# Kernel optimization log

Hardware: AMD Instinct MI355X
Metric: run time of the kernel (lower is better)

Reference implementation:

```python
import jax, jax.numpy as jnp
import numpy as np

P = 10          # num_vars (agents)
DIM = 2         # out_dims (2D)
K = 5           # order
H = 256         # hidden_layer_size
INPUT_DIM = 40  # per-agent feature block
ND = DIM + (P - 1) * DIM  # num_dims_model = 20
OUT = ND * DIM            # per-net MLP output = 40
T = 20000


def _gather_idx():
    # per-agent selected features: [pos(dim), relpos (p-1)*dim] (skips vel at offset dim..2*dim)
    base = np.arange(P) * INPUT_DIM
    a = np.arange(DIM)[None, :] + base[:, None]                      # (P, dim)
    b = np.arange(2 * DIM, (2 + P - 1) * DIM)[None, :] + base[:, None]  # (P, (p-1)*dim)
    return np.concatenate([a, b], axis=1)  # (P, ND)


def _fp_idx():
    i = np.arange(P)[:, None]
    j = np.arange(P - 1)[None, :]
    indd = (i + 1) * INPUT_DIM - (P - 1) + j        # last (p-1) entries of block i
    indd2 = indd - (P - 1)                          # preceding (p-1) entries
    return indd, indd2


def setup_inputs() -> dict:
    key = jax.random.key(0)
    ks = jax.random.split(key, 8)
    s = 0.05
    return {
        "inputs": jax.random.normal(ks[0], (T, K, P * INPUT_DIM), dtype=jnp.float32),
        "W1": jax.random.normal(ks[1], (K, P, ND, H), dtype=jnp.float32) * s,
        "b1": jnp.zeros((K, P, H), dtype=jnp.float32),
        "W2": jax.random.normal(ks[2], (K, P, H, H), dtype=jnp.float32) * s,
        "b2": jnp.zeros((K, P, H), dtype=jnp.float32),
        "W3": jax.random.normal(ks[3], (K, P, H, OUT), dtype=jnp.float32) * s,
        "b3": jnp.zeros((K, P, OUT), dtype=jnp.float32),
        "avoid": jnp.asarray(0.1, dtype=jnp.float32),  # avoid_nets.bias (bat init)
    }


def reference(inputs, W1, b1, W2, b2, W3, b3, avoid):
    Tl = inputs.shape[0]
    idx = _gather_idx()
    indd, indd2 = _fp_idx()

    # pairwise perceptual gating, 'bat' branch (uses avoid bias)
    xlast = inputs[:, -1, :]                       # (T, P*INPUT_DIM)
    xF = xlast[:, indd]                            # (T, P, P-1)
    xF2 = xlast[:, indd2]                          # (T, P, P-1)
    coeffs_FP = jax.nn.sigmoid(100.0 * (xF - avoid)) * (jax.nn.sigmoid(100.0 * xF2) - 0.5) * 2.0

    # grouped per-(k,i) MLPs, batched via einsum
    sel = inputs[:, :, idx]                        # (T, K, P, ND)
    h = jax.nn.relu(jnp.einsum('tkpn,kpnh->tkph', sel, W1) + b1)
    h = jax.nn.relu(jnp.einsum('tkph,kphg->tkpg', h, W2) + b2)
    c = jnp.einsum('tkpg,kpgo->tkpo', h, W3) + b3  # (T, K, P, OUT)
    c = (c ** 2).reshape(Tl, K, P, DIM, ND)        # percept: squared coeffs

    # gate last (p-1)*dim coefficient columns by coeffs_FP (repeated dim times)
    gate = jnp.repeat(coeffs_FP, DIM, axis=-1)     # (T, P, (P-1)*DIM)
    mult = jnp.concatenate([jnp.ones((Tl, P, DIM), dtype=c.dtype), gate], axis=-1)  # (T, P, ND)
    c2 = c * mult[:, None, :, None, :]             # (T, K, P, DIM, ND)

    preds = jnp.einsum('tkpon,tkpn->tpo', c2, sel).reshape(Tl, P * DIM)
    coeffs = c2.reshape(Tl, K, P * DIM, ND)
    return preds, coeffs, coeffs_FP
```

## Files before the change

kernel.cpp:

```cpp
#include <hip/hip_runtime.h>
#include <hip/hip_bf16.h>

#define Kn   5
#define Pn   10
#define Hn   256
#define NDn  20
#define OUTn 40
#define INDn 40
#define ROWn 400
#define TT   32
#define CSTRIDE 52

typedef float  f32x4  __attribute__((ext_vector_type(4)));
typedef float  f32x2  __attribute__((ext_vector_type(2)));
typedef short  bf16x8 __attribute__((ext_vector_type(8)));
typedef unsigned int u32;
typedef unsigned short u16;

#define W1B_OFF 0
#define W1B_PER 8192
#define W2B_OFF 409600
#define W2B_PER 65536
#define W3B_OFF 3686400
#define W3B_PER 12288
#define WS_ELEMS 4300800
#define WS_BYTES (WS_ELEMS * 2)

__device__ __forceinline__ u16 f2bf(float f) {
    u32 u = __float_as_uint(f);
    return (u16)((u + 0x7fffu + ((u >> 16) & 1u)) >> 16);
}

__device__ __forceinline__ u32 cvt_pk_bf16(float a, float b) {
    u32 r;
    asm("v_cvt_pk_bf16_f32 %0, %1, %2" : "=v"(r) : "v"(a), "v"(b));
    return r;
}

__global__ void prep_weights(const float* __restrict__ W1, const float* __restrict__ W2,
                             const float* __restrict__ W3, const float* __restrict__ inputs,
                             const float* __restrict__ avoid_p,
                             float* __restrict__ cfp, short* __restrict__ ws, int T) {
    int sid = blockIdx.x * 256 + threadIdx.x;
    const float* src; int e, kst, n, ss, kmax, ng, nmax; size_t obase;
    if (sid < 51200) {
        e = sid >> 10; int r = sid & 1023; n = r >> 2; ss = r & 3; kst = 0;
        src = W1 + (size_t)e * (NDn * Hn); kmax = NDn; ng = Hn; nmax = Hn;
        obase = W1B_OFF + (size_t)e * W1B_PER;
    } else if (sid < 460800) {
        int s = sid - 51200; e = s >> 13; int r = s & 8191;
        kst = r >> 10; int rr = r & 1023; n = rr >> 2; ss = rr & 3;
        src = W2 + (size_t)e * (Hn * Hn); kmax = Hn; ng = Hn; nmax = Hn;
        obase = W2B_OFF + (size_t)e * W2B_PER + (size_t)kst * 8192;
    } else if (sid < 537600) {
        int s = sid - 460800; e = s / 1536; int r = s - e * 1536;
        kst = r / 192; int rr = r - kst * 192; n = rr >> 2; ss = rr & 3;
        src = W3 + (size_t)e * (Hn * OUTn); kmax = Hn; ng = OUTn; nmax = OUTn;
        obase = W3B_OFF + (size_t)e * W3B_PER + (size_t)kst * 1536;
    } else {
        int g = sid - 537600;
        if (g < T * (Pn * (Pn - 1))) {
            int t = g / 90, rm = g - t * 90;
            int pp = rm / 9, j = rm - pp * 9;
            size_t base = ((size_t)t * Kn + (Kn - 1)) * ROWn + pp * INDn;
            float xF  = inputs[base + 31 + j];
            float xF2 = inputs[base + 22 + j];
            float s1 = 1.0f / (1.0f + __expf(-100.0f * (xF - *avoid_p)));
            float s2 = 1.0f / (1.0f + __expf(-100.0f * xF2));
            cfp[g] = s1 * (s2 - 0.5f) * 2.0f;
        }
        return;
    }

    u16 v[8];
    #pragma unroll
    for (int j = 0; j < 8; ++j) {
        int k = kst * 32 + ss * 8 + j;
        float f = (k < kmax && n < nmax) ? src[(size_t)k * ng + n] : 0.0f;
        v[j] = f2bf(f);
    }
    u32 q0 = (u32)v[0] | ((u32)v[1] << 16), q1 = (u32)v[2] | ((u32)v[3] << 16);
    u32 q2 = (u32)v[4] | ((u32)v[5] << 16), q3 = (u32)v[6] | ((u32)v[7] << 16);
    *(uint4*)(ws + obase + (size_t)n * 32 + ss * 8) = make_uint4(q0, q1, q2, q3);
}

__device__ __forceinline__ void epi_store_h(short* hA_, const f32x4 (*A)[4],
                                            int wid, int lane) {
    const int lg = lane >> 4, lr = lane & 15;
    #pragma unroll
    for (int mt = 0; mt < 2; ++mt) {
        #pragma unroll
        for (int r = 0; r < 4; ++r) {
            const int t = 16 * mt + 4 * lg + r;
            #pragma unroll
            for (int nt = 0; nt < 4; ++nt) {
                float vv = fmaxf(A[mt][nt][r], 0.0f);
                u32 pk = cvt_pk_bf16(vv, vv);
                int col = 64 * wid + 16 * nt + lr;
                int off = t * 512 + ((2 * col) ^ ((t & 7) << 4));
                *reinterpret_cast<u16*>(reinterpret_cast<char*>(hA_) + off) = (u16)pk;
            }
        }
    }
}

template<int KS>
__device__ __forceinline__ void c_step(const char* w2, const short* hA_, int wid,
                                       int lg, int lr, bf16x8 (&cur)[4], bf16x8 (&nxt)[4],
                                       f32x4 (&acc)[2][4]) {
    if (KS < 7) {
        #pragma unroll
        for (int nt = 0; nt < 4; ++nt) {
            int n = 64 * wid + 16 * nt + lr;
            nxt[nt] = *(const bf16x8*)(w2 + (KS + 1) * 16384 + n * 64 + lg * 16);
        }
    }
    bf16x8 aF[2];
    #pragma unroll
    for (int mt = 0; mt < 2; ++mt) {
        int t = 16 * mt + lr;
        aF[mt] = *(const bf16x8*)((const char*)hA_ + t * 512 + ((KS * 64 + lg * 16) ^ ((t & 7) << 4)));
    }
    #pragma unroll
    for (int mt = 0; mt < 2; ++mt)
        #pragma unroll
        for (int nt = 0; nt < 4; ++nt)
            acc[mt][nt] = __builtin_amdgcn_mfma_f32_16x16x32_bf16(aF[mt], cur[nt], acc[mt][nt], 0, 0, 0);
}

template<int KS>
__device__ __forceinline__ void d_step(const char* w3, const short* hA_, int t, int ncnt,
                                       int nbase, int lg, int lr,
                                       bf16x8 (&cur)[2], bf16x8 (&nxt)[2], f32x4 (&accd)[2]) {
    if (KS < 7) {
        #pragma unroll
        for (int j = 0; j < 2; ++j)
            if (j < ncnt) {
                int n = 16 * (nbase + j) + lr;
                nxt[j] = *(const bf16x8*)(w3 + (KS + 1) * 3072 + n * 64 + lg * 16);
            }
    }
    bf16x8 aF = *(const bf16x8*)((const char*)hA_ + t * 512 + ((KS * 64 + lg * 16) ^ ((t & 7) << 4)));
    #pragma unroll
    for (int j = 0; j < 2; ++j)
        if (j < ncnt)
            accd[j] = __builtin_amdgcn_mfma_f32_16x16x32_bf16(aF, cur[j], accd[j], 0, 0, 0);
}

__launch_bounds__(256, 4)
__global__ void senngc_mfma(const float* __restrict__ inputs,
                            const float* __restrict__ b1, const float* __restrict__ b2,
                            const float* __restrict__ b3,
                            const float* __restrict__ cfp_in,
                            const short* __restrict__ ws,
                            float* __restrict__ preds, float* __restrict__ coeffs, int T)
{
    __shared__ __align__(16) short selA[TT * 32];
    __shared__ __align__(16) short hA[TT * Hn];
    __shared__ u16  sh_mult[TT][NDn];

    const int tid  = threadIdx.x;

    const int NB   = gridDim.x;
    const int nch  = NB / (Pn * Kn);
    const int bx   = blockIdx.x & 7, bj = blockIdx.x >> 3;
    const int bbase = NB >> 3, brem = NB & 7;
    const int L    = bx * bbase + (bx < brem ? bx : brem) + bj;
    const int pair = L / nch;
    const int t0   = (L - pair * nch) * TT;
    const int p    = pair / Kn;
    const int ke   = pair - p * Kn;

    const int wid  = tid >> 6, lane = tid & 63;
    const int lg   = lane >> 4, lr = lane & 15;

    const int e = ke * Pn + p;
    const char* w1 = (const char*)(ws + W1B_OFF + (size_t)e * W1B_PER);
    const char* w2 = (const char*)(ws + W2B_OFF + (size_t)e * W2B_PER);
    const char* w3 = (const char*)(ws + W3B_OFF + (size_t)e * W3B_PER);

    if (tid < 128) {
        int row = tid >> 2, ss = tid & 3;
        int kg = ss ^ ((row >> 1) & 3);
        int trow = (t0 + row < T) ? (t0 + row) : (T - 1);
        const float* src = inputs + ((size_t)trow * Kn + ke) * ROWn + p * INDn;
        int c0 = kg ? (kg * 8 + 2) : 0;
        int o1 = kg ? (c0 + 2) : 4;
        int o2 = kg ? (c0 + 4) : 6;
        int o3 = kg ? (c0 + 6) : 8;
        f32x2 va = *(const f32x2*)(src + c0);
        f32x2 vb = *(const f32x2*)(src + o1);
        f32x2 vc = *(const f32x2*)(src + o2);
        f32x2 vd = *(const f32x2*)(src + o3);
        float f[8] = {va[0], va[1], vb[0], vb[1], vc[0], vc[1], vd[0], vd[1]};
        #pragma unroll
        for (int j = 0; j < 8; ++j)
            if (kg * 8 + j >= NDn) f[j] = 0.0f;
        u32 q0 = cvt_pk_bf16(f[0], f[1]), q1 = cvt_pk_bf16(f[2], f[3]);
        u32 q2 = cvt_pk_bf16(f[4], f[5]), q3 = cvt_pk_bf16(f[6], f[7]);
        *(uint4*)((char*)selA + row * 64 + ss * 16) = make_uint4(q0, q1, q2, q3);
    }

    if (tid < 32) *(u32*)&sh_mult[tid][0] = 0x3F803F80u;
    {
        int r = tid / 9, j = tid - r * 9;
        if (tid < TT * (Pn - 1)) {
            float cf = (t0 + r < T) ? cfp_in[(size_t)(t0 + r) * (Pn * (Pn - 1)) + p * (Pn - 1) + j] : 0.0f;
            *(u32*)&sh_mult[r][2 + 2 * j] = cvt_pk_bf16(cf, cf);
        }
        int i2 = tid + 256;
        if (i2 < TT * (Pn - 1)) {
            int r2 = i2 / 9, j2 = i2 - r2 * 9;
            float cf = (t0 + r2 < T) ? cfp_in[(size_t)(t0 + r2) * (Pn * (Pn - 1)) + p * (Pn - 1) + j2] : 0.0f;
            *(u32*)&sh_mult[r2][2 + 2 * j2] = cvt_pk_bf16(cf, cf);
        }
    }

    bf16x8 bW[4];
    float bias1[4], bias2[4];
    #pragma unroll
    for (int nt = 0; nt < 4; ++nt) {
        int n = 64 * wid + 16 * nt + lr;
        bW[nt] = *(const bf16x8*)(w1 + n * 64 + lg * 16);
        bias1[nt] = b1[e * Hn + n];
        bias2[nt] = b2[e * Hn + n];
    }
    __syncthreads();

    f32x4 acc[2][4];

    #pragma unroll
    for (int mt = 0; mt < 2; ++mt)
        #pragma unroll
        for (int nt = 0; nt < 4; ++nt)
            acc[mt][nt] = (f32x4){bias1[nt], bias1[nt], bias1[nt], bias1[nt]};
    {
        bf16x8 aS[2];
        #pragma unroll
        for (int mt = 0; mt < 2; ++mt) {
            int t = 16 * mt + lr;
            aS[mt] = *(const bf16x8*)((const char*)selA + t * 64 + ((lg ^ ((t >> 1) & 3)) << 4));
        }
        #pragma unroll
        for (int mt = 0; mt < 2; ++mt)
            #pragma unroll
            for (int nt = 0; nt < 4; ++nt)
                acc[mt][nt] = __builtin_amdgcn_mfma_f32_16x16x32_bf16(aS[mt], bW[nt], acc[mt][nt], 0, 0, 0);
    }
    bf16x8 bA[4], bB[4];
    #pragma unroll
    for (int nt = 0; nt < 4; ++nt) {
        int n = 64 * wid + 16 * nt + lr;
        bA[nt] = *(const bf16x8*)(w2 + n * 64 + lg * 16);
    }
    epi_store_h(hA, acc, wid, lane);
    __syncthreads();

    #pragma unroll
    for (int mt = 0; mt < 2; ++mt)
        #pragma unroll
        for (int nt = 0; nt < 4; ++nt)
            acc[mt][nt] = (f32x4){bias2[nt], bias2[nt], bias2[nt], bias2[nt]};
    c_step<0>(w2, hA, wid, lg, lr, bA, bB, acc);
    c_step<1>(w2, hA, wid, lg, lr, bB, bA, acc);
    c_step<2>(w2, hA, wid, lg, lr, bA, bB, acc);
    c_step<3>(w2, hA, wid, lg, lr, bB, bA, acc);
    c_step<4>(w2, hA, wid, lg, lr, bA, bB, acc);
    c_step<5>(w2, hA, wid, lg, lr, bB, bA, acc);
    c_step<6>(w2, hA, wid, lg, lr, bA, bB, acc);
    c_step<7>(w2, hA, wid, lg, lr, bB, bA, acc);
    __syncthreads();

    const int mslot = wid >> 1;
    const int nbase = (wid & 1) ? 2 : 0;
    const int ncnt  = (wid & 1) ? 1 : 2;
    const int tD    = 16 * mslot + lr;
    bf16x8 dA[2], dB[2];
    #pragma unroll
    for (int j = 0; j < 2; ++j)
        if (j < ncnt) {
            int n = 16 * (nbase + j) + lr;
            dA[j] = *(const bf16x8*)(w3 + n * 64 + lg * 16);
        }
    epi_store_h(hA, acc, wid, lane);
    __syncthreads();

    {
        f32x4 accd[2];
        accd[0] = (f32x4){0.f, 0.f, 0.f, 0.f};
        accd[1] = (f32x4){0.f, 0.f, 0.f, 0.f};
        d_step<0>(w3, hA, tD, ncnt, nbase, lg, lr, dA, dB, accd);
        d_step<1>(w3, hA, tD, ncnt, nbase, lg, lr, dB, dA, accd);
        d_step<2>(w3, hA, tD, ncnt, nbase, lg, lr, dA, dB, accd);
        d_step<3>(w3, hA, tD, ncnt, nbase, lg, lr, dB, dA, accd);
        d_step<4>(w3, hA, tD, ncnt, nbase, lg, lr, dA, dB, accd);
        d_step<5>(w3, hA, tD, ncnt, nbase, lg, lr, dB, dA, accd);
        d_step<6>(w3, hA, tD, ncnt, nbase, lg, lr, dA, dB, accd);
        d_step<7>(w3, hA, tD, ncnt, nbase, lg, lr, dB, dA, accd);
        __syncthreads();
        {
            float* cst = (float*)hA;
            #pragma unroll
            for (int j = 0; j < 2; ++j)
                if (j < ncnt)
                    #pragma unroll
                    for (int r = 0; r < 4; ++r)
                        cst[(16 * mslot + 4 * lg + r) * CSTRIDE + 16 * (nbase + j) + lr] = accd[j][r];
        }
    }
    __syncthreads();

    {
        const float* cst = (const float*)hA;
        const int r  = tid >> 3, g = tid & 7;
        const int d  = g >> 2;
        const int o0 = 5 * g;
        const int n0 = 5 * (g & 3);
        float s = 0.0f;
        if (t0 + r < T) {
            const float* bb3 = b3 + e * OUTn + o0;
            float* crow = coeffs + (((size_t)(t0 + r) * Kn + ke) * Pn + p) * OUTn + o0;
            #pragma unroll
            for (int j = 0; j < 5; ++j) {
                float c = cst[r * CSTRIDE + o0 + j] + bb3[j];
                int n = n0 + j;
                float m = __uint_as_float((u32)sh_mult[r][n] << 16);
                float c2 = c * c * m;
                crow[j] = c2;
                int offs = r * 64 + (((n >> 3) ^ ((r >> 1) & 3)) << 4) + (n & 7) * 2;
                u16 u = *(const u16*)((const char*)selA + offs);
                s = fmaf(c2, __uint_as_float((u32)u << 16), s);
            }
        }
        s += __shfl_xor(s, 1);
        s += __shfl_xor(s, 2);
        if ((g & 3) == 0 && t0 + r < T)
            atomicAdd(&preds[(size_t)(t0 + r) * (Pn * 2) + p * 2 + d], s);
    }
}

#define FMA4(ACC, A, W)              \
    ACC.x = fmaf(A.x, W, ACC.x);     \
    ACC.y = fmaf(A.y, W, ACC.y);     \
    ACC.z = fmaf(A.z, W, ACC.z);     \
    ACC.w = fmaf(A.w, W, ACC.w);

__launch_bounds__(256, 4)
__global__ void senngc_fused_f32(const float* __restrict__ inputs,
                                 const float* __restrict__ W1, const float* __restrict__ b1,
                                 const float* __restrict__ W2, const float* __restrict__ b2,
                                 const float* __restrict__ W3, const float* __restrict__ b3,
                                 const float* __restrict__ avoid_p,
                                 float* __restrict__ preds, float* __restrict__ coeffs,
                                 float* __restrict__ cfp, int T)
{
    __shared__ __align__(16) float lds_T[Hn * 32];
    __shared__ __align__(16) float selT[NDn * 32];
    __shared__ float sh_mult[32][NDn];
    __shared__ float sh_pred[32][2];

    const int tid = threadIdx.x;
    const int p   = blockIdx.y;
    const int t0  = blockIdx.x * 32;
    const float avoid = *avoid_p;

    if (tid < 64) {
        sh_pred[tid >> 1][tid & 1] = 0.0f;
        sh_mult[tid >> 1][tid & 1] = 1.0f;
    }
    for (int i = tid; i < 32 * (Pn - 1); i += 256) {
        int r = i / 9, j = i - r * 9;
        float cf = 0.0f;
        if (t0 + r < T) {
            size_t base = ((size_t)(t0 + r) * Kn + (Kn - 1)) * ROWn + p * INDn;
            float xF  = inputs[base + 31 + j];
            float xF2 = inputs[base + 22 + j];
            float s1 = 1.0f / (1.0f + __expf(-100.0f * (xF - avoid)));
            float s2 = 1.0f / (1.0f + __expf(-100.0f * xF2));
            cf = s1 * (s2 - 0.5f) * 2.0f;
            cfp[(size_t)(t0 + r) * (Pn * (Pn - 1)) + p * (Pn - 1) + j] = cf;
        }
        sh_mult[r][2 + 2 * j] = cf;
        sh_mult[r][3 + 2 * j] = cf;
    }

    const int tr = tid >> 5;
    const int tc = tid & 31;
    float4 acc[8];

    for (int k = 0; k < Kn; ++k) {
        __syncthreads();
        for (int i = tid; i < NDn * 32; i += 256) {
            int n = i >> 5, r = i & 31;
            float v = 0.0f;
            if (t0 + r < T) {
                int col = p * INDn + (n < 2 ? n : n + 2);
                v = inputs[((size_t)(t0 + r) * Kn + k) * ROWn + col];
            }
            selT[n * 32 + r] = v;
        }
        __syncthreads();
        {
            const float* w1 = W1 + (size_t)(k * Pn + p) * NDn * Hn;
            const float* bb = b1 + (k * Pn + p) * Hn;
            float4 bv0 = *(const float4*)(bb + 8 * tc);
            float4 bv1 = *(const float4*)(bb + 8 * tc + 4);
            acc[0] = make_float4(bv0.x, bv0.x, bv0.x, bv0.x);
            acc[1] = make_float4(bv0.y, bv0.y, bv0.y, bv0.y);
            acc[2] = make_float4(bv0.z, bv0.z, bv0.z, bv0.z);
            acc[3] = make_float4(bv0.w, bv0.w, bv0.w, bv0.w);
            acc[4] = make_float4(bv1.x, bv1.x, bv1.x, bv1.x);
            acc[5] = make_float4(bv1.y, bv1.y, bv1.y, bv1.y);
            acc[6] = make_float4(bv1.z, bv1.z, bv1.z, bv1.z);
            acc[7] = make_float4(bv1.w, bv1.w, bv1.w, bv1.w);
            #pragma unroll 4
            for (int kk = 0; kk < NDn; ++kk) {
                float4 a = *(const float4*)&selT[kk * 32 + 4 * tr];
                const float* wr = w1 + kk * Hn + 8 * tc;
                float4 w0  = *(const float4*)(wr);
                float4 w1v = *(const float4*)(wr + 4);
                FMA4(acc[0], a, w0.x);  FMA4(acc[1], a, w0.y);
                FMA4(acc[2], a, w0.z);  FMA4(acc[3], a, w0.w);
                FMA4(acc[4], a, w1v.x); FMA4(acc[5], a, w1v.y);
                FMA4(acc[6], a, w1v.z); FMA4(acc[7], a, w1v.w);
            }
            #pragma unroll
            for (int c = 0; c < 8; ++c) {
                int col = 8 * tc + c;
                float4 v = acc[c];
                v.x = fmaxf(v.x, 0.0f); v.y = fmaxf(v.y, 0.0f);
                v.z = fmaxf(v.z, 0.0f); v.w = fmaxf(v.w, 0.0f);
                *(float4*)&lds_T[col * 32 + ((4 * tr) ^ ((col & 7) << 2))] = v;
            }
        }
        __syncthreads();
        {
            const float* w2 = W2 + (size_t)(k * Pn + p) * Hn * Hn;
            const float* bb = b2 + (k * Pn + p) * Hn;
            float4 bv0 = *(const float4*)(bb + 8 * tc);
            float4 bv1 = *(const float4*)(bb + 8 * tc + 4);
            acc[0] = make_float4(bv0.x, bv0.x, bv0.x, bv0.x);
            acc[1] = make_float4(bv0.y, bv0.y, bv0.y, bv0.y);
            acc[2] = make_float4(bv0.z, bv0.z, bv0.z, bv0.z);
            acc[3] = make_float4(bv0.w, bv0.w, bv0.w, bv0.w);
            acc[4] = make_float4(bv1.x, bv1.x, bv1.x, bv1.x);
            acc[5] = make_float4(bv1.y, bv1.y, bv1.y, bv1.y);
            acc[6] = make_float4(bv1.z, bv1.z, bv1.z, bv1.z);
            acc[7] = make_float4(bv1.w, bv1.w, bv1.w, bv1.w);
            #pragma unroll 2
            for (int kk = 0; kk < Hn; ++kk) {
                float4 a = *(const float4*)&lds_T[kk * 32 + ((4 * tr) ^ ((kk & 7) << 2))];
                const float* wr = w2 + kk * Hn + 8 * tc;
                float4 w0  = *(const float4*)(wr);
                float4 w1v = *(const float4*)(wr + 4);
                FMA4(acc[0], a, w0.x);  FMA4(acc[1], a, w0.y);
                FMA4(acc[2], a, w0.z);  FMA4(acc[3], a, w0.w);
                FMA4(acc[4], a, w1v.x); FMA4(acc[5], a, w1v.y);
                FMA4(acc[6], a, w1v.z); FMA4(acc[7], a, w1v.w);
            }
            __syncthreads();
            #pragma unroll
            for (int c = 0; c < 8; ++c) {
                int col = 8 * tc + c;
                float4 v = acc[c];
                v.x = fmaxf(v.x, 0.0f); v.y = fmaxf(v.y, 0.0f);
                v.z = fmaxf(v.z, 0.0f); v.w = fmaxf(v.w, 0.0f);
                *(float4*)&lds_T[col * 32 + ((4 * tr) ^ ((col & 7) << 2))] = v;
            }
        }
        __syncthreads();
        {
            const int kq  = tid >> 6;
            const int tr2 = (tid >> 3) & 7;
            const int cg  = tid & 7;
            const float* w3 = W3 + (size_t)(k * Pn + p) * Hn * OUTn;
            float accd[4][5];
            #pragma unroll
            for (int a_ = 0; a_ < 4; ++a_)
                #pragma unroll
                for (int j = 0; j < 5; ++j) accd[a_][j] = 0.0f;
            #pragma unroll 2
            for (int kk = kq * 64; kk < kq * 64 + 64; ++kk) {
                float4 a = *(const float4*)&lds_T[kk * 32 + ((4 * tr2) ^ ((kk & 7) << 2))];
                const float* wr = w3 + kk * OUTn + 5 * cg;
                #pragma unroll
                for (int j = 0; j < 5; ++j) {
                    float w = wr[j];
                    accd[0][j] = fmaf(a.x, w, accd[0][j]);
                    accd[1][j] = fmaf(a.y, w, accd[1][j]);
                    accd[2][j] = fmaf(a.z, w, accd[2][j]);
                    accd[3][j] = fmaf(a.w, w, accd[3][j]);
                }
            }
            __syncthreads();
            #pragma unroll
            for (int r4 = 0; r4 < 4; ++r4)
                #pragma unroll
                for (int j = 0; j < 5; ++j)
                    lds_T[(kq * 32 + 4 * tr2 + r4) * OUTn + 5 * cg + j] = accd[r4][j];
        }
        __syncthreads();
        {
            const float* bb3 = b3 + (k * Pn + p) * OUTn;
            for (int i = tid; i < 32 * OUTn; i += 256) {
                int r = i / OUTn, o = i - r * OUTn;
                if (t0 + r >= T) continue;
                float c = bb3[o]
                        + lds_T[(0 * 32 + r) * OUTn + o]
                        + lds_T[(1 * 32 + r) * OUTn + o]
                        + lds_T[(2 * 32 + r) * OUTn + o]
                        + lds_T[(3 * 32 + r) * OUTn + o];
                int d = (o >= NDn) ? 1 : 0;
                int n = o - d * NDn;
                float c2 = c * c * sh_mult[r][n];
                coeffs[(((size_t)(t0 + r) * Kn + k) * Pn + p) * OUTn + o] = c2;
                atomicAdd(&sh_pred[r][d], c2 * selT[n * 32 + r]);
            }
        }
    }

    __syncthreads();
    if (tid < 64) {
        int r = tid >> 1, d = tid & 1;
        if (t0 + r < T)
            preds[(size_t)(t0 + r) * (Pn * 2) + p * 2 + d] = sh_pred[r][d];
    }
}

extern "C" void kernel_launch(void* const* d_in, const int* in_sizes, int n_in,
                              void* d_out, int out_size, void* d_ws, size_t ws_size,
                              hipStream_t stream) {
    const float* inputs = (const float*)d_in[0];
    const float* W1 = (const float*)d_in[1];
    const float* b1 = (const float*)d_in[2];
    const float* W2 = (const float*)d_in[3];
    const float* b2 = (const float*)d_in[4];
    const float* W3 = (const float*)d_in[5];
    const float* b3 = (const float*)d_in[6];
    const float* avoid = (const float*)d_in[7];
    const int T = in_sizes[0] / (Kn * ROWn);

    float* out    = (float*)d_out;
    float* preds  = out;
    float* coeffs = out + (size_t)T * (Pn * 2);
    float* cfp    = coeffs + (size_t)T * Kn * Pn * OUTn;

    if (ws_size >= (size_t)WS_BYTES) {
        short* ws = (short*)d_ws;
        hipMemsetAsync(preds, 0, (size_t)T * (Pn * 2) * sizeof(float), stream);
        const int prep_items = 537600 + T * (Pn * (Pn - 1));
        hipLaunchKernelGGL(prep_weights, dim3((prep_items + 255) / 256), dim3(256), 0, stream,
                           W1, W2, W3, inputs, avoid, cfp, ws, T);
        const int nch = (T + TT - 1) / TT;
        hipLaunchKernelGGL(senngc_mfma, dim3(nch * Pn * Kn), dim3(256), 0, stream,
                           inputs, b1, b2, b3, cfp, ws, preds, coeffs, T);
    } else {
        dim3 grid((T + 31) / 32, Pn);
        hipLaunchKernelGGL(senngc_fused_f32, grid, dim3(256), 0, stream,
                           inputs, W1, b1, W2, b2, W3, b3, avoid, preds, coeffs, cfp, T);
    }
}
```

Measured before the change: 445.9 us.

## Double time tile to 64 rows with 8 waves sharing each weight load

Raises the per-block time tile from 32 to 64 rows and the block from 256 to 512 threads. The 8 waves are split into two row halves and four column quarters, so each block's weight slices are used for twice as many rows and the number of blocks is halved. This is meant to cut redundant W1/W2/W3 global/L2 traffic per output row. In exchange it doubles shared memory for hA and selA, which may lower occupancy, and the layer-3/epilogue wave mapping (mslot = wid>>1) was not visibly updated for 8 waves.

```diff
diff --git a/kernel.cpp b/kernel.cpp
--- a/kernel.cpp
+++ b/kernel.cpp
@@ -8,7 +8,7 @@
 #define OUTn 40
 #define INDn 40
 #define ROWn 400
-#define TT   32
+#define TT   64
 #define CSTRIDE 52
 
 typedef float  f32x4  __attribute__((ext_vector_type(4)));
@@ -85,18 +85,18 @@
 }
 
 __device__ __forceinline__ void epi_store_h(short* hA_, const f32x4 (*A)[4],
-                                            int wid, int lane) {
+                                            int mh, int nq, int lane) {
     const int lg = lane >> 4, lr = lane & 15;
     #pragma unroll
     for (int mt = 0; mt < 2; ++mt) {
         #pragma unroll
         for (int r = 0; r < 4; ++r) {
-            const int t = 16 * mt + 4 * lg + r;
+            const int t = 32 * mh + 16 * mt + 4 * lg + r;
             #pragma unroll
             for (int nt = 0; nt < 4; ++nt) {
                 float vv = fmaxf(A[mt][nt][r], 0.0f);
                 u32 pk = cvt_pk_bf16(vv, vv);
-                int col = 64 * wid + 16 * nt + lr;
+                int col = 64 * nq + 16 * nt + lr;
                 int off = t * 512 + ((2 * col) ^ ((t & 7) << 4));
                 *reinterpret_cast<u16*>(reinterpret_cast<char*>(hA_) + off) = (u16)pk;
             }
@@ -105,20 +105,20 @@
 }
 
 template<int KS>
-__device__ __forceinline__ void c_step(const char* w2, const short* hA_, int wid,
+__device__ __forceinline__ void c_step(const char* w2, const short* hA_, int mh, int nq,
                                        int lg, int lr, bf16x8 (&cur)[4], bf16x8 (&nxt)[4],
                                        f32x4 (&acc)[2][4]) {
     if (KS < 7) {
         #pragma unroll
         for (int nt = 0; nt < 4; ++nt) {
-            int n = 64 * wid + 16 * nt + lr;
+            int n = 64 * nq + 16 * nt + lr;
             nxt[nt] = *(const bf16x8*)(w2 + (KS + 1) * 16384 + n * 64 + lg * 16);
         }
     }
     bf16x8 aF[2];
     #pragma unroll
     for (int mt = 0; mt < 2; ++mt) {
-        int t = 16 * mt + lr;
+        int t = 32 * mh + 16 * mt + lr;
         aF[mt] = *(const bf16x8*)((const char*)hA_ + t * 512 + ((KS * 64 + lg * 16) ^ ((t & 7) << 4)));
     }
     #pragma unroll
@@ -147,7 +147,7 @@
             accd[j] = __builtin_amdgcn_mfma_f32_16x16x32_bf16(aF, cur[j], accd[j], 0, 0, 0);
 }
 
-__launch_bounds__(256, 4)
+__launch_bounds__(512, 4)
 __global__ void senngc_mfma(const float* __restrict__ inputs,
                             const float* __restrict__ b1, const float* __restrict__ b2,
                             const float* __restrict__ b3,
@@ -173,13 +173,14 @@
 
     const int wid  = tid >> 6, lane = tid & 63;
     const int lg   = lane >> 4, lr = lane & 15;
+    const int mh   = wid >> 2, nq = wid & 3;
 
     const int e = ke * Pn + p;
     const char* w1 = (const char*)(ws + W1B_OFF + (size_t)e * W1B_PER);
     const char* w2 = (const char*)(ws + W2B_OFF + (size_t)e * W2B_PER);
     const char* w3 = (const char*)(ws + W3B_OFF + (size_t)e * W3B_PER);
 
-    if (tid < 128) {
+    if (tid < 256) {
         int row = tid >> 2, ss = tid & 3;
         int kg = ss ^ ((row >> 1) & 3);
         int trow = (t0 + row < T) ? (t0 + row) : (T - 1);
@@ -201,14 +202,14 @@
         *(uint4*)((char*)selA + row * 64 + ss * 16) = make_uint4(q0, q1, q2, q3);
     }
 
-    if (tid < 32) *(u32*)&sh_mult[tid][0] = 0x3F803F80u;
+    if (tid < TT) *(u32*)&sh_mult[tid][0] = 0x3F803F80u;
     {
         int r = tid / 9, j = tid - r * 9;
         if (tid < TT * (Pn - 1)) {
             float cf = (t0 + r < T) ? cfp_in[(size_t)(t0 + r) * (Pn * (Pn - 1)) + p * (Pn - 1) + j] : 0.0f;
             *(u32*)&sh_mult[r][2 + 2 * j] = cvt_pk_bf16(cf, cf);
         }
-        int i2 = tid + 256;
+        int i2 = tid + 512;
         if (i2 < TT * (Pn - 1)) {
             int r2 = i2 / 9, j2 = i2 - r2 * 9;
             float cf = (t0 + r2 < T) ? cfp_in[(size_t)(t0 + r2) * (Pn * (Pn - 1)) + p * (Pn - 1) + j2] : 0.0f;
@@ -220,7 +221,7 @@
     float bias1[4], bias2[4];
     #pragma unroll
     for (int nt = 0; nt < 4; ++nt) {
-        int n = 64 * wid + 16 * nt + lr;
+        int n = 64 * nq + 16 * nt + lr;
         bW[nt] = *(const bf16x8*)(w1 + n * 64 + lg * 16);
         bias1[nt] = b1[e * Hn + n];
         bias2[nt] = b2[e * Hn + n];
@@ -238,7 +239,7 @@
         bf16x8 aS[2];
         #pragma unroll
         for (int mt = 0; mt < 2; ++mt) {
-            int t = 16 * mt + lr;
+            int t = 32 * mh + 16 * mt + lr;
             aS[mt] = *(const bf16x8*)((const char*)selA + t * 64 + ((lg ^ ((t >> 1) & 3)) << 4));
         }
         #pragma unroll
@@ -250,10 +251,10 @@
     bf16x8 bA[4], bB[4];
     #pragma unroll
     for (int nt = 0; nt < 4; ++nt) {
-        int n = 64 * wid + 16 * nt + lr;
+        int n = 64 * nq + 16 * nt + lr;
         bA[nt] = *(const bf16x8*)(w2 + n * 64 + lg * 16);
     }
-    epi_store_h(hA, acc, wid, lane);
+    epi_store_h(hA, acc, mh, nq, lane);
     __syncthreads();
 
     #pragma unroll
@@ -261,14 +262,14 @@
         #pragma unroll
         for (int nt = 0; nt < 4; ++nt)
             acc[mt][nt] = (f32x4){bias2[nt], bias2[nt], bias2[nt], bias2[nt]};
-    c_step<0>(w2, hA, wid, lg, lr, bA, bB, acc);
-    c_step<1>(w2, hA, wid, lg, lr, bB, bA, acc);
-    c_step<2>(w2, hA, wid, lg, lr, bA, bB, acc);
-    c_step<3>(w2, hA, wid, lg, lr, bB, bA, acc);
-    c_step<4>(w2, hA, wid, lg, lr, bA, bB, acc);
-    c_step<5>(w2, hA, wid, lg, lr, bB, bA, acc);
-    c_step<6>(w2, hA, wid, lg, lr, bA, bB, acc);
-    c_step<7>(w2, hA, wid, lg, lr, bB, bA, acc);
+    c_step<0>(w2, hA, mh, nq, lg, lr, bA, bB, acc);
+    c_step<1>(w2, hA, mh, nq, lg, lr, bB, bA, acc);
+    c_step<2>(w2, hA, mh, nq, lg, lr, bA, bB, acc);
+    c_step<3>(w2, hA, mh, nq, lg, lr, bB, bA, acc);
+    c_step<4>(w2, hA, mh, nq, lg, lr, bA, bB, acc);
+    c_step<5>(w2, hA, mh, nq, lg, lr, bB, bA, acc);
+    c_step<6>(w2, hA, mh, nq, lg, lr, bA, bB, acc);
+    c_step<7>(w2, hA, mh, nq, lg, lr, bB, bA, acc);
     __syncthreads();
 
     const int mslot = wid >> 1;
@@ -282,7 +283,7 @@
             int n = 16 * (nbase + j) + lr;
             dA[j] = *(const bf16x8*)(w3 + n * 64 + lg * 16);
         }
-    epi_store_h(hA, acc, wid, lane);
+    epi_store_h(hA, acc, mh, nq, lane);
     __syncthreads();
 
     {
@@ -552,7 +553,7 @@
         hipLaunchKernelGGL(prep_weights, dim3((prep_items + 255) / 256), dim3(256), 0, stream,
                            W1, W2, W3, inputs, avoid, cfp, ws, T);
         const int nch = (T + TT - 1) / TT;
-        hipLaunchKernelGGL(senngc_mfma, dim3(nch * Pn * Kn), dim3(256), 0, stream,
+        hipLaunchKernelGGL(senngc_mfma, dim3(nch * Pn * Kn), dim3(512), 0, stream,
                            inputs, b1, b2, b3, cfp, ws, preds, coeffs, T);
     } else {
         dim3 grid((T + 31) / 32, Pn);
```

Result: slower. 466.2 us (+4.6%).
